# Performance work log

Measured on AMD Instinct MI355X. Metric: run time of the kernel, lower is better.

## Reference

```python
import jax, jax.numpy as jnp
import numpy as np

HIDDEN = 2048
NUM_HEADS = 16
NUM_KV_HEADS = 4
HEAD_DIM = HIDDEN // NUM_HEADS  # 128
GROUP = NUM_HEADS // NUM_KV_HEADS  # 4
SCALE = HEAD_DIM ** -0.5


def setup_inputs() -> dict:
    key = jax.random.key(0)
    ks = jax.random.split(key, 9)
    B, S = 2, 2048
    kv_dim = HEAD_DIM * NUM_KV_HEADS
    std = HIDDEN ** -0.5
    return {
        "x": jax.random.normal(ks[0], (B, S, HIDDEN), dtype=jnp.float32),
        "Wq": jax.random.normal(ks[1], (HIDDEN, HIDDEN), dtype=jnp.float32) * std,
        "bq": jnp.zeros((HIDDEN,), dtype=jnp.float32),
        "Wk": jax.random.normal(ks[2], (HIDDEN, kv_dim), dtype=jnp.float32) * std,
        "bk": jnp.zeros((kv_dim,), dtype=jnp.float32),
        "Wv": jax.random.normal(ks[3], (HIDDEN, kv_dim), dtype=jnp.float32) * std,
        "bv": jnp.zeros((kv_dim,), dtype=jnp.float32),
        "Wo": jax.random.normal(ks[4], (HIDDEN, HIDDEN), dtype=jnp.float32) * std,
        "bo": jnp.zeros((HIDDEN,), dtype=jnp.float32),
    }


def reference(x, Wq, bq, Wk, bk, Wv, bv, Wo, bo):
    B, S, _ = x.shape
    # projections
    q = (x @ Wq + bq).reshape(B, S, NUM_KV_HEADS, GROUP, HEAD_DIM)  # grouped query heads
    k = (x @ Wk + bk).reshape(B, S, NUM_KV_HEADS, HEAD_DIM)
    v = (x @ Wv + bv).reshape(B, S, NUM_KV_HEADS, HEAD_DIM)
    # scores: [B, Hkv, G, Sq, Sk] -- same math as repeat_interleave of K/V over G,
    # but K/V are broadcast over the group axis instead of materialized.
    attn = jnp.einsum("bqhgd,bkhd->bhgqk", q, k) * SCALE
    attn = jax.nn.softmax(attn, axis=-1)
    out = jnp.einsum("bhgqk,bkhd->bqhgd", attn, v).reshape(B, S, HIDDEN)
    return out @ Wo + bo
```

## Files before the change

kernel.cpp:

```cpp
#include <hip/hip_runtime.h>


#define SEQ    2048
#define HIDDEN 2048
#define NKV    4
#define HD     128

typedef __attribute__((ext_vector_type(8))) short v8s;
typedef __attribute__((ext_vector_type(4))) float v4f;

#define MFMA16(a,b,c) __builtin_amdgcn_mfma_f32_16x16x32_bf16((a),(b),(c),0,0,0)

__device__ __forceinline__ ushort f2b(float f){
  unsigned u = __float_as_uint(f);
  u += 0x7fffu + ((u >> 16) & 1u);
  return (ushort)(u >> 16);
}

__device__ __forceinline__ void gload16(const void* g, void* l){
  __builtin_amdgcn_global_load_lds((const __attribute__((address_space(1))) void*)g,
                                   (__attribute__((address_space(3))) void*)l, 16, 0, 0);
}

__global__ void k_conv(const float* __restrict__ in, ushort* __restrict__ out, int n){
  int i = (blockIdx.x*256 + threadIdx.x)*4;
  if (i >= n) return;
  float4 f = *(const float4*)(in + i);
  ushort4 u; u.x=f2b(f.x); u.y=f2b(f.y); u.z=f2b(f.z); u.w=f2b(f.w);
  *(ushort4*)(out + i) = u;
}

__global__ void k_tconv(const float* __restrict__ in, ushort* __restrict__ out,
                        int rows, int cols){
  __shared__ float t[32][33];
  int tx = threadIdx.x & 31, ty = threadIdx.x >> 5;
  int c0 = blockIdx.x*32, r0 = blockIdx.y*32;
#pragma unroll
  for (int i=0;i<4;i++) t[ty+i*8][tx] = in[(size_t)(r0+ty+i*8)*cols + c0+tx];
  __syncthreads();
#pragma unroll
  for (int i=0;i<4;i++) out[(size_t)(c0+ty+i*8)*rows + r0+tx] = f2b(t[tx][ty+i*8]);
}

__global__ void k_tv(const ushort* __restrict__ vb, ushort* __restrict__ vT){
  __shared__ ushort t[32][33];
  int tx = threadIdx.x & 31, ty = threadIdx.x >> 5;
  int s0 = blockIdx.x*32, d0 = blockIdx.y*32, bh = blockIdx.z;
  int b = bh >> 2, h = bh & 3;
  const ushort* src = vb + (size_t)b*SEQ*512 + h*128;
#pragma unroll
  for (int i=0;i<4;i++) t[ty+i*8][tx] = src[(size_t)(s0+ty+i*8)*512 + d0+tx];
  __syncthreads();
  ushort* dst = vT + (size_t)bh*128*SEQ;
#pragma unroll
  for (int i=0;i<4;i++) dst[(size_t)(d0+ty+i*8)*SEQ + s0+tx] = t[tx][ty+i*8];
}


#define GEMM_MAIN(A_, Bt_, K_)                                                        \
  __shared__ ushort sA[128*32], sB[128*32];                                           \
  const int tid = threadIdx.x, lane = tid & 63, wid = tid >> 6;                       \
  const int wm = wid >> 1, wn = wid & 1, lm = lane & 15, q8 = (lane >> 4)*8;          \
  const int rowB = blockIdx.y*128, colB = blockIdx.x*128;                             \
  v4f acc[4][4] = {};                                                                 \
  for (int k0 = 0; k0 < (K_); k0 += 32){                                              \
    _Pragma("unroll")                                                                 \
    for (int it=0; it<2; it++){                                                       \
      int c = tid + it*256;                                                           \
      gload16((A_)  + (size_t)(rowB + (c>>2))*(K_) + k0 + (c&3)*8, (char*)sA + c*16); \
      gload16((Bt_) + (size_t)(colB + (c>>2))*(K_) + k0 + (c&3)*8, (char*)sB + c*16); \
    }                                                                                 \
    __syncthreads();                                                                  \
    v8s af[4], bfr[4];                                                                \
    _Pragma("unroll")                                                                 \
    for (int i=0;i<4;i++){                                                            \
      af[i]  = *(const v8s*)(sA + (wm*64 + i*16 + lm)*32 + q8);                       \
      bfr[i] = *(const v8s*)(sB + (wn*64 + i*16 + lm)*32 + q8);                       \
    }                                                                                 \
    _Pragma("unroll")                                                                 \
    for (int i=0;i<4;i++)                                                             \
      _Pragma("unroll")                                                               \
      for (int j=0;j<4;j++) acc[i][j] = MFMA16(af[i], bfr[j], acc[i][j]);             \
    __syncthreads();                                                                  \
  }                                                                                   \
  const int quad = lane >> 4;

__global__ __launch_bounds__(256) void k_gemm_qkv(
    const ushort* __restrict__ A, const ushort* __restrict__ Bt,
    const float* __restrict__ bq, const float* __restrict__ bk, const float* __restrict__ bv,
    ushort* __restrict__ qb, ushort* __restrict__ kb, ushort* __restrict__ vb){
  GEMM_MAIN(A, Bt, HIDDEN)
#pragma unroll
  for (int i=0;i<4;i++)
#pragma unroll
  for (int j=0;j<4;j++){
    int col = colB + wn*64 + j*16 + lm;
#pragma unroll
    for (int r=0;r<4;r++){
      int row = rowB + wm*64 + i*16 + quad*4 + r;
      float v = acc[i][j][r];
      if (col < 2048)      qb[(size_t)row*2048 + col]        = f2b(v + bq[col]);
      else if (col < 2560) kb[(size_t)row*512 + (col-2048)]  = f2b(v + bk[col-2048]);
      else                 vb[(size_t)row*512 + (col-2560)]  = f2b(v + bv[col-2560]);
    }
  }
}

__global__ __launch_bounds__(256) void k_gemm_out(
    const ushort* __restrict__ A, const ushort* __restrict__ Bt,
    const float* __restrict__ bo, float* __restrict__ out){
  GEMM_MAIN(A, Bt, HIDDEN)
#pragma unroll
  for (int i=0;i<4;i++)
#pragma unroll
  for (int j=0;j<4;j++){
    int col = colB + wn*64 + j*16 + lm;
#pragma unroll
    for (int r=0;r<4;r++){
      int row = rowB + wm*64 + i*16 + quad*4 + r;
      out[(size_t)row*2048 + col] = acc[i][j][r] + bo[col];
    }
  }
}

#define ATS 136

__global__ __launch_bounds__(256) void k_attn(
    const ushort* __restrict__ qb, const ushort* __restrict__ kb,
    const ushort* __restrict__ vT, ushort* __restrict__ Ob){
  __shared__ ushort sK[128*ATS];
  __shared__ ushort sV[128*ATS];
  const int tid = threadIdx.x, lane = tid & 63, w = tid >> 6;
  const int lm = lane & 15, quad = lane >> 4, q8 = quad*8;
  const int qt = blockIdx.x, head = blockIdx.y, b = blockIdx.z;
  const int hkv = head >> 2;
  const float C = 0.08838834764831845f * 1.4426950408889634f;

  v8s qf[2][4];
#pragma unroll
  for (int rb=0; rb<2; rb++)
#pragma unroll
    for (int ks=0; ks<4; ks++)
      qf[rb][ks] = *(const v8s*)(qb + (size_t)(b*SEQ + qt*128 + w*32 + rb*16 + lm)*HIDDEN
                                    + head*HD + ks*32 + q8);

  v4f o[2][8] = {};
  float mreg[2] = {-3e38f, -3e38f};
  float lreg[2] = {0.f, 0.f};

  for (int t=0; t<SEQ/128; t++){
    __syncthreads();
    const int kt0 = t*128;
#pragma unroll
    for (int it=0; it<8; it++){
      int c = tid + it*256, r = c >> 4, cw = (c & 15)*8;
      *(int4*)(sK + r*ATS + cw) = *(const int4*)(kb + (size_t)(b*SEQ + kt0 + r)*512 + hkv*HD + cw);
      *(int4*)(sV + r*ATS + cw) = *(const int4*)(vT + (size_t)((b*NKV + hkv)*HD + r)*SEQ + kt0 + cw);
    }
    __syncthreads();

    v4f sacc[2][8] = {};
#pragma unroll
    for (int ct=0; ct<8; ct++){
      v8s kf[4];
#pragma unroll
      for (int ks=0; ks<4; ks++) kf[ks] = *(const v8s*)(sK + (ct*16 + lm)*ATS + ks*32 + q8);
#pragma unroll
      for (int rb=0; rb<2; rb++)
#pragma unroll
        for (int ks=0; ks<4; ks++) sacc[rb][ct] = MFMA16(kf[ks], qf[rb][ks], sacc[rb][ct]);
    }
    __syncthreads();

    float alpha[2];
#pragma unroll
    for (int rb=0; rb<2; rb++){
      float mx = mreg[rb];
#pragma unroll
      for (int ct=0; ct<8; ct++)
#pragma unroll
        for (int r=0;r<4;r++) mx = fmaxf(mx, sacc[rb][ct][r]);
      mx = fmaxf(mx, __shfl_xor(mx, 16));
      mx = fmaxf(mx, __shfl_xor(mx, 32));
      alpha[rb] = __builtin_amdgcn_exp2f((mreg[rb]-mx)*C);
      mreg[rb] = mx;
      float rs = 0.f;
      ushort* prow = sK + (size_t)(w*32 + rb*16 + lm)*ATS;
#pragma unroll
      for (int ct=0; ct<8; ct++){
        float p0 = __builtin_amdgcn_exp2f((sacc[rb][ct][0]-mx)*C);
        float p1 = __builtin_amdgcn_exp2f((sacc[rb][ct][1]-mx)*C);
        float p2 = __builtin_amdgcn_exp2f((sacc[rb][ct][2]-mx)*C);
        float p3 = __builtin_amdgcn_exp2f((sacc[rb][ct][3]-mx)*C);
        rs += (p0+p1)+(p2+p3);
        uint2 pk;
        pk.x = (unsigned)f2b(p0) | ((unsigned)f2b(p1) << 16);
        pk.y = (unsigned)f2b(p2) | ((unsigned)f2b(p3) << 16);
        *(uint2*)(prow + ct*16 + quad*4) = pk;
      }
      rs += __shfl_xor(rs, 16);
      rs += __shfl_xor(rs, 32);
      lreg[rb] = lreg[rb]*alpha[rb] + rs;
    }

#pragma unroll
    for (int rbo=0; rbo<2; rbo++)
#pragma unroll
      for (int r=0;r<4;r++){
        float a = __shfl(alpha[rbo], (lane & 48) + quad*4 + r);
#pragma unroll
        for (int dt=0; dt<8; dt++) o[rbo][dt][r] *= a;
      }

    v8s pa[2][4];
#pragma unroll
    for (int rbo=0; rbo<2; rbo++)
#pragma unroll
      for (int ks2=0; ks2<4; ks2++)
        pa[rbo][ks2] = *(const v8s*)(sK + (size_t)(w*32 + rbo*16 + lm)*ATS + ks2*32 + q8);
#pragma unroll
    for (int dt=0; dt<8; dt++){
      v8s vf[4];
#pragma unroll
      for (int ks2=0; ks2<4; ks2++) vf[ks2] = *(const v8s*)(sV + (dt*16 + lm)*ATS + ks2*32 + q8);
#pragma unroll
      for (int rbo=0; rbo<2; rbo++)
#pragma unroll
        for (int ks2=0; ks2<4; ks2++) o[rbo][dt] = MFMA16(pa[rbo][ks2], vf[ks2], o[rbo][dt]);
    }
  }

#pragma unroll
  for (int rbo=0; rbo<2; rbo++){
    float inv[4];
#pragma unroll
    for (int r=0;r<4;r++) inv[r] = 1.0f / __shfl(lreg[rbo], (lane & 48) + quad*4 + r);
#pragma unroll
    for (int dt=0; dt<8; dt++)
#pragma unroll
      for (int r=0;r<4;r++){
        int row = b*SEQ + qt*128 + w*32 + rbo*16 + quad*4 + r;
        int col = head*HD + dt*16 + lm;
        Ob[(size_t)row*HIDDEN + col] = f2b(o[rbo][dt][r]*inv[r]);
      }
  }
}

extern "C" void kernel_launch(void* const* d_in, const int* in_sizes, int n_in,
                              void* d_out, int out_size, void* d_ws, size_t ws_size,
                              hipStream_t stream){
  const float* x  = (const float*)d_in[0];
  const float* Wq = (const float*)d_in[1];
  const float* bq = (const float*)d_in[2];
  const float* Wk = (const float*)d_in[3];
  const float* bk = (const float*)d_in[4];
  const float* Wv = (const float*)d_in[5];
  const float* bv = (const float*)d_in[6];
  const float* Wo = (const float*)d_in[7];
  const float* bo = (const float*)d_in[8];
  float* out = (float*)d_out;

  ushort* xb  = (ushort*)d_ws;
  ushort* Wt  = xb  + 8388608;
  ushort* Wto = Wt  + 6291456;
  ushort* qb  = Wto + 4194304;
  ushort* kb  = qb  + 8388608;
  ushort* vb  = kb  + 2097152;
  ushort* vT  = vb  + 2097152;
  ushort* Ob  = vT  + 2097152;

  k_conv <<<8192, 256, 0, stream>>>(x, xb, 8388608);
  k_tconv<<<dim3(64,64), 256, 0, stream>>>(Wq, Wt, 2048, 2048);
  k_tconv<<<dim3(16,64), 256, 0, stream>>>(Wk, Wt + 4194304, 2048, 512);
  k_tconv<<<dim3(16,64), 256, 0, stream>>>(Wv, Wt + 5242880, 2048, 512);
  k_tconv<<<dim3(64,64), 256, 0, stream>>>(Wo, Wto, 2048, 2048);
  k_gemm_qkv<<<dim3(24,32), 256, 0, stream>>>(xb, Wt, bq, bk, bv, qb, kb, vb);
  k_tv  <<<dim3(64,4,8), 256, 0, stream>>>(vb, vT);
  k_attn<<<dim3(16,16,2), 256, 0, stream>>>(qb, kb, vT, Ob);
  k_gemm_out<<<dim3(16,32), 256, 0, stream>>>(Ob, Wto, bo, out);
}
```

Baseline: 380.7 us.

## Write K/V in MFMA fragment layout and run single-wave attention blocks

The QKV GEMM epilogue now scatters K and V straight into a pre-swizzled fragment layout, so the separate V transpose kernel is dropped. Attention becomes one wave per block covering 32 query rows, with 32-key tiles brought into LDS through direct global-to-LDS loads and s_waitcnt in place of block barriers. Each fragment is then read with a single contiguous 16-byte LDS load. The aim is to cut a launch and a pass over V, remove padded LDS indexing and barriers, and raise the block count. The cost is scattered 2-byte stores in the GEMM epilogue and loads that are not overlapped with compute within a wave.

```diff
diff --git a/kernel.cpp b/kernel.cpp
--- a/kernel.cpp
+++ b/kernel.cpp
@@ -3,8 +3,6 @@
 
 #define SEQ    2048
 #define HIDDEN 2048
-#define NKV    4
-#define HD     128
 
 typedef __attribute__((ext_vector_type(8))) short v8s;
 typedef __attribute__((ext_vector_type(4))) float v4f;
@@ -21,6 +19,9 @@
   __builtin_amdgcn_global_load_lds((const __attribute__((address_space(1))) void*)g,
                                    (__attribute__((address_space(3))) void*)l, 16, 0, 0);
 }
+
+#define WAIT_VM0   0x0F70
+#define WAIT_LGKM0 0xC07F
 
 __global__ void k_conv(const float* __restrict__ in, ushort* __restrict__ out, int n){
   int i = (blockIdx.x*256 + threadIdx.x)*4;
@@ -41,21 +42,6 @@
 #pragma unroll
   for (int i=0;i<4;i++) out[(size_t)(c0+ty+i*8)*rows + r0+tx] = f2b(t[tx][ty+i*8]);
 }
-
-__global__ void k_tv(const ushort* __restrict__ vb, ushort* __restrict__ vT){
-  __shared__ ushort t[32][33];
-  int tx = threadIdx.x & 31, ty = threadIdx.x >> 5;
-  int s0 = blockIdx.x*32, d0 = blockIdx.y*32, bh = blockIdx.z;
-  int b = bh >> 2, h = bh & 3;
-  const ushort* src = vb + (size_t)b*SEQ*512 + h*128;
-#pragma unroll
-  for (int i=0;i<4;i++) t[ty+i*8][tx] = src[(size_t)(s0+ty+i*8)*512 + d0+tx];
-  __syncthreads();
-  ushort* dst = vT + (size_t)bh*128*SEQ;
-#pragma unroll
-  for (int i=0;i<4;i++) dst[(size_t)(d0+ty+i*8)*SEQ + s0+tx] = t[tx][ty+i*8];
-}
-
 
 #define GEMM_MAIN(A_, Bt_, K_)                                                        \
   __shared__ ushort sA[128*32], sB[128*32];                                           \
@@ -88,7 +74,7 @@
 __global__ __launch_bounds__(256) void k_gemm_qkv(
     const ushort* __restrict__ A, const ushort* __restrict__ Bt,
     const float* __restrict__ bq, const float* __restrict__ bk, const float* __restrict__ bv,
-    ushort* __restrict__ qb, ushort* __restrict__ kb, ushort* __restrict__ vb){
+    ushort* __restrict__ qb, ushort* __restrict__ kbF, ushort* __restrict__ vbF){
   GEMM_MAIN(A, Bt, HIDDEN)
 #pragma unroll
   for (int i=0;i<4;i++)
@@ -98,10 +84,23 @@
 #pragma unroll
     for (int r=0;r<4;r++){
       int row = rowB + wm*64 + i*16 + quad*4 + r;
+      int b = row >> 11, s = row & 2047;
       float v = acc[i][j][r];
-      if (col < 2048)      qb[(size_t)row*2048 + col]        = f2b(v + bq[col]);
-      else if (col < 2560) kb[(size_t)row*512 + (col-2048)]  = f2b(v + bk[col-2048]);
-      else                 vb[(size_t)row*512 + (col-2560)]  = f2b(v + bv[col-2560]);
+      if (col < 2048){
+        qb[(size_t)row*2048 + col] = f2b(v + bq[col]);
+      } else if (col < 2560){
+        int c = col - 2048, hkv = c >> 7, d = c & 127;
+        size_t a = (size_t)(b*4+hkv)*262144 + (size_t)(s>>5)*4096
+                 + (size_t)((((s>>4)&1)*4) + (d>>5))*512
+                 + (size_t)((((d>>3)&3)*16 + (s&15))*8) + (d&7);
+        kbF[a] = f2b(v + bk[c]);
+      } else {
+        int c = col - 2560, hkv = c >> 7, d = c & 127;
+        size_t a = (size_t)(b*4+hkv)*262144 + (size_t)(s>>5)*4096
+                 + (size_t)(d>>4)*512
+                 + (size_t)((((s>>3)&3)*16 + (d&15))*8) + (s&7);
+        vbF[a] = f2b(v + bv[c]);
+      }
     }
   }
 }
@@ -123,80 +122,79 @@
   }
 }
 
-#define ATS 136
-
-__global__ __launch_bounds__(256) void k_attn(
-    const ushort* __restrict__ qb, const ushort* __restrict__ kb,
-    const ushort* __restrict__ vT, ushort* __restrict__ Ob){
-  __shared__ ushort sK[128*ATS];
-  __shared__ ushort sV[128*ATS];
-  const int tid = threadIdx.x, lane = tid & 63, w = tid >> 6;
+__global__ __launch_bounds__(64,2) void k_attn(
+    const ushort* __restrict__ qb, const ushort* __restrict__ kbF,
+    const ushort* __restrict__ vbF, ushort* __restrict__ Ob){
+  __shared__ ushort sK[4096];
+  __shared__ ushort sV[4096];
+  const int lane = threadIdx.x;
   const int lm = lane & 15, quad = lane >> 4, q8 = quad*8;
   const int qt = blockIdx.x, head = blockIdx.y, b = blockIdx.z;
   const int hkv = head >> 2;
   const float C = 0.08838834764831845f * 1.4426950408889634f;
 
+  const ushort* kbase = kbF + (size_t)(b*4+hkv)*262144;
+  const ushort* vbase = vbF + (size_t)(b*4+hkv)*262144;
+
   v8s qf[2][4];
 #pragma unroll
   for (int rb=0; rb<2; rb++)
 #pragma unroll
     for (int ks=0; ks<4; ks++)
-      qf[rb][ks] = *(const v8s*)(qb + (size_t)(b*SEQ + qt*128 + w*32 + rb*16 + lm)*HIDDEN
-                                    + head*HD + ks*32 + q8);
+      qf[rb][ks] = *(const v8s*)(qb + (size_t)(b*SEQ + qt*32 + rb*16 + lm)*HIDDEN
+                                    + head*128 + ks*32 + q8);
 
   v4f o[2][8] = {};
   float mreg[2] = {-3e38f, -3e38f};
   float lreg[2] = {0.f, 0.f};
 
-  for (int t=0; t<SEQ/128; t++){
-    __syncthreads();
-    const int kt0 = t*128;
-#pragma unroll
-    for (int it=0; it<8; it++){
-      int c = tid + it*256, r = c >> 4, cw = (c & 15)*8;
-      *(int4*)(sK + r*ATS + cw) = *(const int4*)(kb + (size_t)(b*SEQ + kt0 + r)*512 + hkv*HD + cw);
-      *(int4*)(sV + r*ATS + cw) = *(const int4*)(vT + (size_t)((b*NKV + hkv)*HD + r)*SEQ + kt0 + cw);
-    }
-    __syncthreads();
-
-    v4f sacc[2][8] = {};
-#pragma unroll
-    for (int ct=0; ct<8; ct++){
+  for (int t2=0; t2<64; t2++){
+    __builtin_amdgcn_s_waitcnt(WAIT_LGKM0);
+    const ushort* kc = kbase + t2*4096;
+    const ushort* vc = vbase + t2*4096;
+#pragma unroll
+    for (int c=0; c<8; c++) gload16(kc + c*512 + lane*8, sK + c*512 + lane*8);
+#pragma unroll
+    for (int c=0; c<8; c++) gload16(vc + c*512 + lane*8, sV + c*512 + lane*8);
+    __builtin_amdgcn_s_waitcnt(WAIT_VM0);
+
+    v4f sacc[2][2] = {};
+#pragma unroll
+    for (int ct=0; ct<2; ct++){
       v8s kf[4];
 #pragma unroll
-      for (int ks=0; ks<4; ks++) kf[ks] = *(const v8s*)(sK + (ct*16 + lm)*ATS + ks*32 + q8);
+      for (int ks=0; ks<4; ks++) kf[ks] = *(const v8s*)(sK + (ct*4+ks)*512 + lane*8);
 #pragma unroll
       for (int rb=0; rb<2; rb++)
 #pragma unroll
         for (int ks=0; ks<4; ks++) sacc[rb][ct] = MFMA16(kf[ks], qf[rb][ks], sacc[rb][ct]);
     }
-    __syncthreads();
 
     float alpha[2];
 #pragma unroll
     for (int rb=0; rb<2; rb++){
       float mx = mreg[rb];
 #pragma unroll
-      for (int ct=0; ct<8; ct++)
+      for (int ct=0; ct<2; ct++)
 #pragma unroll
         for (int r=0;r<4;r++) mx = fmaxf(mx, sacc[rb][ct][r]);
       mx = fmaxf(mx, __shfl_xor(mx, 16));
       mx = fmaxf(mx, __shfl_xor(mx, 32));
       alpha[rb] = __builtin_amdgcn_exp2f((mreg[rb]-mx)*C);
       mreg[rb] = mx;
-      float rs = 0.f;
-      ushort* prow = sK + (size_t)(w*32 + rb*16 + lm)*ATS;
-#pragma unroll
-      for (int ct=0; ct<8; ct++){
-        float p0 = __builtin_amdgcn_exp2f((sacc[rb][ct][0]-mx)*C);
-        float p1 = __builtin_amdgcn_exp2f((sacc[rb][ct][1]-mx)*C);
-        float p2 = __builtin_amdgcn_exp2f((sacc[rb][ct][2]-mx)*C);
-        float p3 = __builtin_amdgcn_exp2f((sacc[rb][ct][3]-mx)*C);
+      float mxC = mx*C, rs = 0.f;
+#pragma unroll
+      for (int ct=0; ct<2; ct++){
+        float p0 = __builtin_amdgcn_exp2f(fmaf(sacc[rb][ct][0], C, -mxC));
+        float p1 = __builtin_amdgcn_exp2f(fmaf(sacc[rb][ct][1], C, -mxC));
+        float p2 = __builtin_amdgcn_exp2f(fmaf(sacc[rb][ct][2], C, -mxC));
+        float p3 = __builtin_amdgcn_exp2f(fmaf(sacc[rb][ct][3], C, -mxC));
         rs += (p0+p1)+(p2+p3);
         uint2 pk;
         pk.x = (unsigned)f2b(p0) | ((unsigned)f2b(p1) << 16);
         pk.y = (unsigned)f2b(p2) | ((unsigned)f2b(p3) << 16);
-        *(uint2*)(prow + ct*16 + quad*4) = pk;
+        int dstlane = (ct*2 + (quad>>1))*16 + lm;
+        *(uint2*)(sK + rb*512 + dstlane*8 + (quad&1)*4) = pk;
       }
       rs += __shfl_xor(rs, 16);
       rs += __shfl_xor(rs, 32);
@@ -212,21 +210,15 @@
         for (int dt=0; dt<8; dt++) o[rbo][dt][r] *= a;
       }
 
-    v8s pa[2][4];
-#pragma unroll
-    for (int rbo=0; rbo<2; rbo++)
-#pragma unroll
-      for (int ks2=0; ks2<4; ks2++)
-        pa[rbo][ks2] = *(const v8s*)(sK + (size_t)(w*32 + rbo*16 + lm)*ATS + ks2*32 + q8);
+    __builtin_amdgcn_s_waitcnt(WAIT_LGKM0);
+    v8s pa[2];
+#pragma unroll
+    for (int rb=0; rb<2; rb++) pa[rb] = *(const v8s*)(sK + rb*512 + lane*8);
 #pragma unroll
     for (int dt=0; dt<8; dt++){
-      v8s vf[4];
-#pragma unroll
-      for (int ks2=0; ks2<4; ks2++) vf[ks2] = *(const v8s*)(sV + (dt*16 + lm)*ATS + ks2*32 + q8);
-#pragma unroll
-      for (int rbo=0; rbo<2; rbo++)
-#pragma unroll
-        for (int ks2=0; ks2<4; ks2++) o[rbo][dt] = MFMA16(pa[rbo][ks2], vf[ks2], o[rbo][dt]);
+      v8s vf = *(const v8s*)(sV + dt*512 + lane*8);
+#pragma unroll
+      for (int rbo=0; rbo<2; rbo++) o[rbo][dt] = MFMA16(pa[rbo], vf, o[rbo][dt]);
     }
   }
 
@@ -239,8 +231,8 @@
     for (int dt=0; dt<8; dt++)
 #pragma unroll
       for (int r=0;r<4;r++){
-        int row = b*SEQ + qt*128 + w*32 + rbo*16 + quad*4 + r;
-        int col = head*HD + dt*16 + lm;
+        int row = b*SEQ + qt*32 + rbo*16 + quad*4 + r;
+        int col = head*128 + dt*16 + lm;
         Ob[(size_t)row*HIDDEN + col] = f2b(o[rbo][dt][r]*inv[r]);
       }
   }
@@ -264,18 +256,16 @@
   ushort* Wt  = xb  + 8388608;
   ushort* Wto = Wt  + 6291456;
   ushort* qb  = Wto + 4194304;
-  ushort* kb  = qb  + 8388608;
-  ushort* vb  = kb  + 2097152;
-  ushort* vT  = vb  + 2097152;
-  ushort* Ob  = vT  + 2097152;
+  ushort* kbF = qb  + 8388608;
+  ushort* vbF = kbF + 2097152;
+  ushort* Ob  = vbF + 2097152;
 
   k_conv <<<8192, 256, 0, stream>>>(x, xb, 8388608);
   k_tconv<<<dim3(64,64), 256, 0, stream>>>(Wq, Wt, 2048, 2048);
   k_tconv<<<dim3(16,64), 256, 0, stream>>>(Wk, Wt + 4194304, 2048, 512);
   k_tconv<<<dim3(16,64), 256, 0, stream>>>(Wv, Wt + 5242880, 2048, 512);
   k_tconv<<<dim3(64,64), 256, 0, stream>>>(Wo, Wto, 2048, 2048);
-  k_gemm_qkv<<<dim3(24,32), 256, 0, stream>>>(xb, Wt, bq, bk, bv, qb, kb, vb);
-  k_tv  <<<dim3(64,4,8), 256, 0, stream>>>(vb, vT);
-  k_attn<<<dim3(16,16,2), 256, 0, stream>>>(qb, kb, vT, Ob);
+  k_gemm_qkv<<<dim3(24,32), 256, 0, stream>>>(xb, Wt, bq, bk, bv, qb, kbF, vbF);
+  k_attn<<<dim3(64,16,2), 64, 0, stream>>>(qb, kbF, vbF, Ob);
   k_gemm_out<<<dim3(16,32), 256, 0, stream>>>(Ob, Wto, bo, out);
 }
```

New measurement: 431.8 us. 13.4% more time.

## Restructure attention into single-wave blocks with register-prefetched K/V tiles

Applied to the files above, without the earlier changes.

The attention kernel becomes one 64-lane wave per block, each handling 32 query rows. It loads K and V fragments directly from global memory into registers, double-buffering K across 32-key steps. This removes the shared-memory K/V staging and the block-wide barriers. Only a small shared buffer is kept to reshape P into MFMA operand layout. The grid orders blocks so the four query heads sharing a KV head sit next to each other for cache reuse. The trade-off is no cross-wave K/V sharing through LDS, more global/L2 traffic, higher register pressure, and shorter MFMA chains per softmax step.

```diff
diff --git a/kernel.cpp b/kernel.cpp
--- a/kernel.cpp
+++ b/kernel.cpp
@@ -3,8 +3,6 @@
 
 #define SEQ    2048
 #define HIDDEN 2048
-#define NKV    4
-#define HD     128
 
 typedef __attribute__((ext_vector_type(8))) short v8s;
 typedef __attribute__((ext_vector_type(4))) float v4f;
@@ -55,7 +53,6 @@
 #pragma unroll
   for (int i=0;i<4;i++) dst[(size_t)(d0+ty+i*8)*SEQ + s0+tx] = t[tx][ty+i*8];
 }
-
 
 #define GEMM_MAIN(A_, Bt_, K_)                                                        \
   __shared__ ushort sA[128*32], sB[128*32];                                           \
@@ -123,80 +120,74 @@
   }
 }
 
-#define ATS 136
-
-__global__ __launch_bounds__(256) void k_attn(
+__global__ __launch_bounds__(64,2) void k_attn(
     const ushort* __restrict__ qb, const ushort* __restrict__ kb,
     const ushort* __restrict__ vT, ushort* __restrict__ Ob){
-  __shared__ ushort sK[128*ATS];
-  __shared__ ushort sV[128*ATS];
-  const int tid = threadIdx.x, lane = tid & 63, w = tid >> 6;
+  __shared__ ushort sP[1024];
+  const int lane = threadIdx.x;
   const int lm = lane & 15, quad = lane >> 4, q8 = quad*8;
-  const int qt = blockIdx.x, head = blockIdx.y, b = blockIdx.z;
-  const int hkv = head >> 2;
+  const int pair = blockIdx.x & 7, g = blockIdx.x >> 3;
+  const int b = pair >> 2, hkv = pair & 3, head = hkv*4 + g;
+  const int qt = blockIdx.y;
   const float C = 0.08838834764831845f * 1.4426950408889634f;
 
+  const ushort* kbb = kb + (size_t)b*SEQ*512 + hkv*128;
+  const ushort* vbb = vT + (size_t)(b*4+hkv)*128*SEQ;
+
   v8s qf[2][4];
 #pragma unroll
   for (int rb=0; rb<2; rb++)
 #pragma unroll
     for (int ks=0; ks<4; ks++)
-      qf[rb][ks] = *(const v8s*)(qb + (size_t)(b*SEQ + qt*128 + w*32 + rb*16 + lm)*HIDDEN
-                                    + head*HD + ks*32 + q8);
+      qf[rb][ks] = *(const v8s*)(qb + (size_t)(b*SEQ + qt*32 + rb*16 + lm)*HIDDEN
+                                    + head*128 + ks*32 + q8);
 
   v4f o[2][8] = {};
   float mreg[2] = {-3e38f, -3e38f};
   float lreg[2] = {0.f, 0.f};
 
-  for (int t=0; t<SEQ/128; t++){
-    __syncthreads();
-    const int kt0 = t*128;
-#pragma unroll
-    for (int it=0; it<8; it++){
-      int c = tid + it*256, r = c >> 4, cw = (c & 15)*8;
-      *(int4*)(sK + r*ATS + cw) = *(const int4*)(kb + (size_t)(b*SEQ + kt0 + r)*512 + hkv*HD + cw);
-      *(int4*)(sV + r*ATS + cw) = *(const int4*)(vT + (size_t)((b*NKV + hkv)*HD + r)*SEQ + kt0 + cw);
-    }
-    __syncthreads();
-
-    v4f sacc[2][8] = {};
-#pragma unroll
-    for (int ct=0; ct<8; ct++){
-      v8s kf[4];
-#pragma unroll
-      for (int ks=0; ks<4; ks++) kf[ks] = *(const v8s*)(sK + (ct*16 + lm)*ATS + ks*32 + q8);
+  v8s kA[2][4], kB[2][4], vf[8];
+
+#define LOADK(dst, t) { _Pragma("unroll") for (int ct=0; ct<2; ct++)                  \
+    _Pragma("unroll") for (int ks=0; ks<4; ks++)                                      \
+      dst[ct][ks] = *(const v8s*)(kbb + (size_t)((t)*32 + ct*16 + lm)*512 + ks*32 + q8); }
+#define LOADV(t) { _Pragma("unroll") for (int dt=0; dt<8; dt++)                       \
+      vf[dt] = *(const v8s*)(vbb + (size_t)(dt*16 + lm)*SEQ + (t)*32 + q8); }
+
+  auto body = [&](const v8s (&kf)[2][4]){
+    v4f sacc[2][2] = {};
+#pragma unroll
+    for (int ct=0; ct<2; ct++)
 #pragma unroll
       for (int rb=0; rb<2; rb++)
 #pragma unroll
-        for (int ks=0; ks<4; ks++) sacc[rb][ct] = MFMA16(kf[ks], qf[rb][ks], sacc[rb][ct]);
-    }
-    __syncthreads();
+        for (int ks=0; ks<4; ks++) sacc[rb][ct] = MFMA16(kf[ct][ks], qf[rb][ks], sacc[rb][ct]);
 
     float alpha[2];
 #pragma unroll
     for (int rb=0; rb<2; rb++){
       float mx = mreg[rb];
 #pragma unroll
-      for (int ct=0; ct<8; ct++)
+      for (int ct=0; ct<2; ct++)
 #pragma unroll
         for (int r=0;r<4;r++) mx = fmaxf(mx, sacc[rb][ct][r]);
       mx = fmaxf(mx, __shfl_xor(mx, 16));
       mx = fmaxf(mx, __shfl_xor(mx, 32));
       alpha[rb] = __builtin_amdgcn_exp2f((mreg[rb]-mx)*C);
       mreg[rb] = mx;
-      float rs = 0.f;
-      ushort* prow = sK + (size_t)(w*32 + rb*16 + lm)*ATS;
-#pragma unroll
-      for (int ct=0; ct<8; ct++){
-        float p0 = __builtin_amdgcn_exp2f((sacc[rb][ct][0]-mx)*C);
-        float p1 = __builtin_amdgcn_exp2f((sacc[rb][ct][1]-mx)*C);
-        float p2 = __builtin_amdgcn_exp2f((sacc[rb][ct][2]-mx)*C);
-        float p3 = __builtin_amdgcn_exp2f((sacc[rb][ct][3]-mx)*C);
+      float mxC = mx*C, rs = 0.f;
+#pragma unroll
+      for (int ct=0; ct<2; ct++){
+        float p0 = __builtin_amdgcn_exp2f(fmaf(sacc[rb][ct][0], C, -mxC));
+        float p1 = __builtin_amdgcn_exp2f(fmaf(sacc[rb][ct][1], C, -mxC));
+        float p2 = __builtin_amdgcn_exp2f(fmaf(sacc[rb][ct][2], C, -mxC));
+        float p3 = __builtin_amdgcn_exp2f(fmaf(sacc[rb][ct][3], C, -mxC));
         rs += (p0+p1)+(p2+p3);
         uint2 pk;
         pk.x = (unsigned)f2b(p0) | ((unsigned)f2b(p1) << 16);
         pk.y = (unsigned)f2b(p2) | ((unsigned)f2b(p3) << 16);
-        *(uint2*)(prow + ct*16 + quad*4) = pk;
+        int dstlane = (ct*2 + (quad>>1))*16 + lm;
+        *(uint2*)(sP + rb*512 + dstlane*8 + (quad&1)*4) = pk;
       }
       rs += __shfl_xor(rs, 16);
       rs += __shfl_xor(rs, 32);
@@ -212,22 +203,23 @@
         for (int dt=0; dt<8; dt++) o[rbo][dt][r] *= a;
       }
 
-    v8s pa[2][4];
-#pragma unroll
-    for (int rbo=0; rbo<2; rbo++)
-#pragma unroll
-      for (int ks2=0; ks2<4; ks2++)
-        pa[rbo][ks2] = *(const v8s*)(sK + (size_t)(w*32 + rbo*16 + lm)*ATS + ks2*32 + q8);
-#pragma unroll
-    for (int dt=0; dt<8; dt++){
-      v8s vf[4];
-#pragma unroll
-      for (int ks2=0; ks2<4; ks2++) vf[ks2] = *(const v8s*)(sV + (dt*16 + lm)*ATS + ks2*32 + q8);
-#pragma unroll
-      for (int rbo=0; rbo<2; rbo++)
-#pragma unroll
-        for (int ks2=0; ks2<4; ks2++) o[rbo][dt] = MFMA16(pa[rbo][ks2], vf[ks2], o[rbo][dt]);
-    }
+    v8s pa[2];
+#pragma unroll
+    for (int rb=0; rb<2; rb++) pa[rb] = *(const v8s*)(sP + rb*512 + lane*8);
+#pragma unroll
+    for (int dt=0; dt<8; dt++)
+#pragma unroll
+      for (int rbo=0; rbo<2; rbo++) o[rbo][dt] = MFMA16(pa[rbo], vf[dt], o[rbo][dt]);
+  };
+
+  LOADK(kA, 0)
+  for (int t=0; t<64; t+=2){
+    LOADK(kB, t+1)
+    LOADV(t)
+    body(kA);
+    LOADK(kA, (t+2)&63)
+    LOADV(t+1)
+    body(kB);
   }
 
 #pragma unroll
@@ -239,11 +231,13 @@
     for (int dt=0; dt<8; dt++)
 #pragma unroll
       for (int r=0;r<4;r++){
-        int row = b*SEQ + qt*128 + w*32 + rbo*16 + quad*4 + r;
-        int col = head*HD + dt*16 + lm;
+        int row = b*SEQ + qt*32 + rbo*16 + quad*4 + r;
+        int col = head*128 + dt*16 + lm;
         Ob[(size_t)row*HIDDEN + col] = f2b(o[rbo][dt][r]*inv[r]);
       }
   }
+#undef LOADK
+#undef LOADV
 }
 
 extern "C" void kernel_launch(void* const* d_in, const int* in_sizes, int n_in,
@@ -276,6 +270,6 @@
   k_tconv<<<dim3(64,64), 256, 0, stream>>>(Wo, Wto, 2048, 2048);
   k_gemm_qkv<<<dim3(24,32), 256, 0, stream>>>(xb, Wt, bq, bk, bv, qb, kb, vb);
   k_tv  <<<dim3(64,4,8), 256, 0, stream>>>(vb, vT);
-  k_attn<<<dim3(16,16,2), 256, 0, stream>>>(qb, kb, vT, Ob);
+  k_attn<<<dim3(32,64), 64, 0, stream>>>(qb, kb, vT, Ob);
   k_gemm_out<<<dim3(16,32), 256, 0, stream>>>(Ob, Wto, bo, out);
 }
```

Result: slower. 479.3 us (+25.9%).
